# Performance work log

Hardware: AMD Instinct MI355X
Metric: run time of the kernel (lower is better)

Reference implementation:

```python
import jax, jax.numpy as jnp
import numpy as np

N_CELLS = 50000
IN_DIM = 2000
H_DIM = 128
Z_DIM = 64
N_PROTO = 32
N_CLASSES = 8
B = 64  # number of samples (ragged groups)


def _xavier(key, shape):
    fan_out, fan_in = shape
    std = jnp.sqrt(2.0 / (fan_in + fan_out))
    return std * jax.random.normal(key, shape, dtype=jnp.float32)


def setup_inputs() -> dict:
    key = jax.random.key(0)
    ks = jax.random.split(key, 16)
    x = jax.random.normal(ks[0], (N_CELLS, IN_DIM), dtype=jnp.float32)
    y = jax.random.randint(ks[1], (B,), 0, N_CLASSES)
    # sorted segment ids emulating split_idx over B ragged groups; every group non-empty
    seg = jnp.sort(jax.random.randint(ks[2], (N_CELLS - B,), 0, B))
    segment_ids = jnp.sort(jnp.concatenate([jnp.arange(B, dtype=seg.dtype), seg])).astype(jnp.int32)
    return {
        "x": x,
        "y": y,
        "segment_ids": segment_ids,
        "enc_i_w": _xavier(ks[3], (H_DIM, IN_DIM)),
        "enc_i_b": jnp.zeros((H_DIM,), jnp.float32),
        "enc_h0_w": _xavier(ks[4], (H_DIM, H_DIM)),
        "enc_h0_b": jnp.zeros((H_DIM,), jnp.float32),
        "enc_z_w": _xavier(ks[5], (Z_DIM, H_DIM)),
        "enc_z_b": jnp.zeros((Z_DIM,), jnp.float32),
        "imp_i_w": _xavier(ks[6], (H_DIM, IN_DIM)),
        "imp_i_b": jnp.zeros((H_DIM,), jnp.float32),
        "imp_h0_w": _xavier(ks[7], (H_DIM, H_DIM)),
        "imp_h0_b": jnp.zeros((H_DIM,), jnp.float32),
        "imp_p_w": _xavier(ks[8], (N_PROTO * N_CLASSES, H_DIM)),
        "imp_p_b": jnp.zeros((N_PROTO * N_CLASSES,), jnp.float32),
        "prototypes": _xavier(ks[9], (N_PROTO, Z_DIM)),
    }


def _linear(x, w, b):
    # torch nn.Linear: y = x @ w.T + b
    return x @ w.T + b


def reference(x, y, segment_ids,
              enc_i_w, enc_i_b, enc_h0_w, enc_h0_b, enc_z_w, enc_z_b,
              imp_i_w, imp_i_b, imp_h0_w, imp_h0_b, imp_p_w, imp_p_b,
              prototypes):
    act = jax.nn.leaky_relu  # slope 0.01, matches nn.LeakyReLU default
    # encode
    h = act(_linear(x, enc_i_w, enc_i_b))
    h = act(_linear(h, enc_h0_w, enc_h0_b))
    z = act(_linear(h, enc_z_w, enc_z_b))  # [N, Z]
    # importance scores
    hi = act(_linear(x, imp_i_w, imp_i_b))
    hi = act(_linear(hi, imp_h0_w, imp_h0_b))
    imp = jax.nn.sigmoid(_linear(hi, imp_p_w, imp_p_b)).reshape(-1, N_PROTO, N_CLASSES)  # [N, P, C]
    # squared euclidean cell-to-prototype distances [N, P]
    c2p = jnp.sum((z[:, None, :] - prototypes[None, :, :]) ** 2, axis=-1)
    sim = 1.0 / (c2p + 0.5)  # [N, P]
    c_logits = jnp.einsum('np,npc->nc', sim, imp)  # [N, C]
    # ragged per-sample mean (segment mean over split_idx groups)
    sums = jax.ops.segment_sum(c_logits, segment_ids, num_segments=B)
    counts = jax.ops.segment_sum(jnp.ones((c_logits.shape[0],), c_logits.dtype), segment_ids, num_segments=B)
    logits = sums / counts[:, None]  # [B, C]
    # mean cross-entropy
    logp = jax.nn.log_softmax(logits, axis=-1)
    clf_loss = -jnp.mean(jnp.take_along_axis(logp, y[:, None], axis=1))
    total_loss = clf_loss  # ct is None -> ct_loss = 0
    return total_loss, logits
```

## Files before the change

### kernel.cpp

```cpp
#include <hip/hip_runtime.h>
#include <math.h>

#define N_CELLS 50000
#define KDIM    2000
#define KPAD    2048
#define BK      128
#define NCHUNK  16
#define TM      64

typedef unsigned short u16;
typedef unsigned int   u32;
typedef __attribute__((ext_vector_type(8))) short          bf16x8;
typedef __attribute__((ext_vector_type(4))) float          f32x4;
typedef __attribute__((ext_vector_type(4))) unsigned short u16x4;

__device__ __forceinline__ u16 f2bf(float f) {
  u32 u = __builtin_bit_cast(u32, f);
  return (u16)((u + 0x7FFFu + ((u >> 16) & 1u)) >> 16);
}
__device__ __forceinline__ float bf2f(u16 h) {
  u32 u = ((u32)h) << 16;
  return __builtin_bit_cast(float, u);
}

#define WS_W1     0
#define WS_W2     1048576
#define WS_W3     (WS_W2 + 65536)
#define WS_PT     (WS_W3 + 81920)
#define WS_PN     (WS_PT + 4096)
#define WS_B1     (WS_PN + 128)
#define WS_B2     (WS_B1 + 1024)
#define WS_B3     (WS_B2 + 1024)
#define WS_SEGSUM (WS_B3 + 1280)
#define WS_SEGCNT (WS_SEGSUM + 2048)

#define LDS_SEG  0
#define LDS_SA   256
#define LDS_H2   256
#define LDS_SIM  256
#define LDS_H1   34048
#define LDS_IMP  34048
#define LDS_ZB   67840
#define LDS_CL   67840
#define LDS_ZN   77056
#define LDS_TOTAL 77312

__global__ void __launch_bounds__(256) convert_kernel(
    const float* __restrict__ enc_i_w, const float* __restrict__ imp_i_w,
    const float* __restrict__ enc_h0_w, const float* __restrict__ imp_h0_w,
    const float* __restrict__ enc_z_w, const float* __restrict__ imp_p_w,
    const float* __restrict__ protos,
    const float* __restrict__ enc_i_b, const float* __restrict__ imp_i_b,
    const float* __restrict__ enc_h0_b, const float* __restrict__ imp_h0_b,
    const float* __restrict__ enc_z_b, const float* __restrict__ imp_p_b,
    char* __restrict__ ws)
{
  u16* W1 = (u16*)(ws + WS_W1);
  u16* W2 = (u16*)(ws + WS_W2);
  u16* W3 = (u16*)(ws + WS_W3);
  u16* PT = (u16*)(ws + WS_PT);
  float* PN = (float*)(ws + WS_PN);
  float* b1 = (float*)(ws + WS_B1);
  float* b2 = (float*)(ws + WS_B2);
  float* b3 = (float*)(ws + WS_B3);

  int idx = blockIdx.x * 256 + threadIdx.x;
  if (idx < 524288) {
    int r = idx >> 11, k = idx & 2047;
    float v = 0.f;
    if (k < KDIM) v = (r < 128) ? enc_i_w[r * KDIM + k] : imp_i_w[(r - 128) * KDIM + k];
    W1[((k >> 3) * 256 + r) * 8 + (k & 7)] = f2bf(v);
  } else if (idx < 557056) {
    int j = idx - 524288; int r = j >> 7, k = j & 127;
    float v = (r < 128) ? enc_h0_w[r * 128 + k] : imp_h0_w[(r - 128) * 128 + k];
    W2[j] = f2bf(v);
  } else if (idx < 598016) {
    int j = idx - 557056; int r = j >> 7, k = j & 127;
    float v = (r < 64) ? enc_z_w[r * 128 + k] : imp_p_w[(r - 64) * 128 + k];
    W3[j] = f2bf(v);
  } else if (idx < 600064) {
    int j = idx - 598016;
    PT[j] = f2bf(protos[j]);
  } else if (idx < 600096) {
    int p = idx - 600064;
    float s = 0.f;
    for (int d = 0; d < 64; ++d) { float pb = bf2f(f2bf(protos[p * 64 + d])); s += pb * pb; }
    PN[p] = s + 0.5f;
  } else if (idx < 600352) {
    int j = idx - 600096;
    b1[j] = (j < 128) ? enc_i_b[j] : imp_i_b[j - 128];
  } else if (idx < 600608) {
    int j = idx - 600352;
    b2[j] = (j < 128) ? enc_h0_b[j] : imp_h0_b[j - 128];
  } else if (idx < 600928) {
    int j = idx - 600608;
    b3[j] = (j < 64) ? enc_z_b[j] : imp_p_b[j - 64];
  }
}

#define MFMA(a, b, c) __builtin_amdgcn_mfma_f32_16x16x32_bf16((a), (b), (c), 0, 0, 0)
#define LD8(p) (*(const bf16x8*)(const void*)(p))

#define A_GLOAD(t_) {                                                        \
  const int kb_ = (t_) * BK;                                                 \
  _Pragma("unroll")                                                          \
  for (int j_ = 0; j_ < 4; ++j_) {                                           \
    const int col_ = kb_ + (ac + 8 * j_) * 4;                                \
    aR[j_] = (arow_ok && col_ < KDIM)                                        \
               ? __builtin_nontemporal_load((const f32x4*)(xr + col_))       \
               : f4z;                                                        \
  } }

#define A_STORE(buf_) {                                                      \
  u16* da_ = saB + (buf_) * (TM * BK) + ar * BK;                             \
  _Pragma("unroll")                                                          \
  for (int j_ = 0; j_ < 4; ++j_) {                                           \
    u16x4 pk_;                                                               \
    pk_[0] = f2bf(aR[j_][0]); pk_[1] = f2bf(aR[j_][1]);                      \
    pk_[2] = f2bf(aR[j_][2]); pk_[3] = f2bf(aR[j_][3]);                      \
    const int cu_ = ((ac + 8 * j_) * 4) ^ swW;                               \
    *(u16x4*)(void*)(da_ + cu_) = pk_;                                       \
  } }

__global__ void __launch_bounds__(512, 4) fused_main(
    const float* __restrict__ x, const int* __restrict__ seg,
    const char* __restrict__ ws,
    float* __restrict__ seg_sums, float* __restrict__ seg_counts)
{
  extern __shared__ char smem[];
  const int tid  = threadIdx.x;
  const int wave = tid >> 6;
  const int lane = tid & 63;
  const int l15  = lane & 15;
  const int l4   = lane >> 4;
  const int row0 = blockIdx.x * TM;
  int valid = N_CELLS - row0; if (valid > TM) valid = TM;
  const int wn0 = wave * 32;

  if (tid < TM) {
    int r = row0 + tid;
    ((int*)(smem + LDS_SEG))[tid] = (r < N_CELLS) ? seg[r] : 0;
  }

  u16* const saB = (u16*)(smem + LDS_SA);
  const int ar = tid >> 3;
  const int ac = tid & 7;
  const bool arow_ok = (row0 + ar) < N_CELLS;
  const float* xr = x + (size_t)(arow_ok ? (row0 + ar) : 0) * KDIM;
  const u16* const w1t = (const u16*)(ws + WS_W1);
  const u16* const bbase = w1t + (size_t)(l4 * 256 + wn0 + l15) * 8;
  const int swW = (ar & 7) << 3;
  const int swR = (l15 & 7) << 3;
  const f32x4 f4z = (f32x4){0.f, 0.f, 0.f, 0.f};

  f32x4 aR[4];
  f32x4 acc1[4][2];
#pragma unroll
  for (int m = 0; m < 4; ++m)
#pragma unroll
    for (int n = 0; n < 2; ++n) acc1[m][n] = (f32x4){0.f, 0.f, 0.f, 0.f};

  A_GLOAD(0);
  A_STORE(0);
  __syncthreads();

  int cur = 0;
  for (int t = 0; t < NCHUNK; ++t) {
    bf16x8 bR[8];
#pragma unroll
    for (int q = 0; q < 8; ++q)
      bR[q] = LD8(bbase + (size_t)(t * 16 + (q >> 1) * 4) * 2048 + (q & 1) * 128);
    if (t + 1 < NCHUNK) A_GLOAD(t + 1);
    const u16* sa = saB + cur * (TM * BK);
#pragma unroll
    for (int kk = 0; kk < 4; ++kk) {
      const int co = (kk * 32 + l4 * 8) ^ swR;
      bf16x8 af0 = LD8(sa + (l15)      * BK + co);
      bf16x8 af1 = LD8(sa + (16 + l15) * BK + co);
      bf16x8 af2 = LD8(sa + (32 + l15) * BK + co);
      bf16x8 af3 = LD8(sa + (48 + l15) * BK + co);
      acc1[0][0] = MFMA(af0, bR[kk*2+0], acc1[0][0]);
      acc1[0][1] = MFMA(af0, bR[kk*2+1], acc1[0][1]);
      acc1[1][0] = MFMA(af1, bR[kk*2+0], acc1[1][0]);
      acc1[1][1] = MFMA(af1, bR[kk*2+1], acc1[1][1]);
      acc1[2][0] = MFMA(af2, bR[kk*2+0], acc1[2][0]);
      acc1[2][1] = MFMA(af2, bR[kk*2+1], acc1[2][1]);
      acc1[3][0] = MFMA(af3, bR[kk*2+0], acc1[3][0]);
      acc1[3][1] = MFMA(af3, bR[kk*2+1], acc1[3][1]);
    }
    if (t + 1 < NCHUNK) A_STORE(cur ^ 1);
    __syncthreads();
    cur ^= 1;
  }

  u16* h1 = (u16*)(smem + LDS_H1);
  {
    const float* b1 = (const float*)(ws + WS_B1);
#pragma unroll
    for (int n = 0; n < 2; ++n) {
      const int col = wn0 + n * 16 + l15;
      const float bias = b1[col];
#pragma unroll
      for (int m = 0; m < 4; ++m)
#pragma unroll
        for (int j = 0; j < 4; ++j) {
          const int row = m * 16 + l4 * 4 + j;
          float v = acc1[m][n][j] + bias;
          v = (v > 0.f) ? v : 0.01f * v;
          h1[row * 264 + col] = f2bf(v);
        }
    }
  }
  __syncthreads();

  u16* h2 = (u16*)(smem + LDS_H2);
  {
    const u16* W2 = (const u16*)(ws + WS_W2);
    const int branch = wave >> 2;
    f32x4 acc2[4][2];
#pragma unroll
    for (int m = 0; m < 4; ++m)
#pragma unroll
      for (int n = 0; n < 2; ++n) acc2[m][n] = (f32x4){0.f, 0.f, 0.f, 0.f};
#pragma unroll
    for (int kk = 0; kk < 4; ++kk) {
      const int ko = kk * 32 + l4 * 8;
      bf16x8 af[4], bfr[2];
#pragma unroll
      for (int m = 0; m < 4; ++m) af[m] = LD8(h1 + (m * 16 + l15) * 264 + branch * 128 + ko);
#pragma unroll
      for (int n = 0; n < 2; ++n) bfr[n] = LD8(W2 + (wn0 + n * 16 + l15) * 128 + ko);
#pragma unroll
      for (int m = 0; m < 4; ++m)
#pragma unroll
        for (int n = 0; n < 2; ++n) acc2[m][n] = MFMA(af[m], bfr[n], acc2[m][n]);
    }
    const float* b2 = (const float*)(ws + WS_B2);
#pragma unroll
    for (int n = 0; n < 2; ++n) {
      const int col = wn0 + n * 16 + l15;
      const float bias = b2[col];
#pragma unroll
      for (int m = 0; m < 4; ++m)
#pragma unroll
        for (int j = 0; j < 4; ++j) {
          const int row = m * 16 + l4 * 4 + j;
          float v = acc2[m][n][j] + bias;
          v = (v > 0.f) ? v : 0.01f * v;
          h2[row * 264 + col] = f2bf(v);
        }
    }
  }
  __syncthreads();

  {
    const u16* W3 = (const u16*)(ws + WS_W3);
    const float* b3 = (const float*)(ws + WS_B3);
    f32x4 acc3[4][2];
#pragma unroll
    for (int m = 0; m < 4; ++m)
#pragma unroll
      for (int n = 0; n < 2; ++n) acc3[m][n] = (f32x4){0.f, 0.f, 0.f, 0.f};
#pragma unroll
    for (int kk = 0; kk < 4; ++kk) {
      const int ko = kk * 32 + l4 * 8;
      bf16x8 af[4], bfr[2];
#pragma unroll
      for (int m = 0; m < 4; ++m) af[m] = LD8(h2 + (m * 16 + l15) * 264 + 128 + ko);
#pragma unroll
      for (int n = 0; n < 2; ++n) bfr[n] = LD8(W3 + (64 + wn0 + n * 16 + l15) * 128 + ko);
#pragma unroll
      for (int m = 0; m < 4; ++m)
#pragma unroll
        for (int n = 0; n < 2; ++n) acc3[m][n] = MFMA(af[m], bfr[n], acc3[m][n]);
    }
    u16* impL = (u16*)(smem + LDS_IMP);
#pragma unroll
    for (int n = 0; n < 2; ++n) {
      const int col = wn0 + n * 16 + l15;
      const float bias = b3[64 + col];
#pragma unroll
      for (int m = 0; m < 4; ++m)
#pragma unroll
        for (int j = 0; j < 4; ++j) {
          const int row = m * 16 + l4 * 4 + j;
          float v = acc3[m][n][j] + bias;
          impL[row * 264 + col] = f2bf(1.f / (1.f + expf(-v)));
        }
    }
    if (wave < 4) {
      f32x4 accz[4];
#pragma unroll
      for (int n = 0; n < 4; ++n) accz[n] = (f32x4){0.f, 0.f, 0.f, 0.f};
#pragma unroll
      for (int kk = 0; kk < 4; ++kk) {
        const int ko = kk * 32 + l4 * 8;
        bf16x8 a = LD8(h2 + (wave * 16 + l15) * 264 + ko);
#pragma unroll
        for (int n = 0; n < 4; ++n) {
          bf16x8 b = LD8(W3 + (n * 16 + l15) * 128 + ko);
          accz[n] = MFMA(a, b, accz[n]);
        }
      }
      u16* zb = (u16*)(smem + LDS_ZB);
      float zn[4] = {0.f, 0.f, 0.f, 0.f};
#pragma unroll
      for (int n = 0; n < 4; ++n) {
        const int col = n * 16 + l15;
        const float bias = b3[col];
#pragma unroll
        for (int j = 0; j < 4; ++j) {
          const int row = wave * 16 + l4 * 4 + j;
          float v = accz[n][j] + bias;
          v = (v > 0.f) ? v : 0.01f * v;
          zb[row * 72 + col] = f2bf(v);
          zn[j] += v * v;
        }
      }
#pragma unroll
      for (int j = 0; j < 4; ++j) {
        float v = zn[j];
        v += __shfl_xor(v, 1); v += __shfl_xor(v, 2);
        v += __shfl_xor(v, 4); v += __shfl_xor(v, 8);
        zn[j] = v;
      }
      if (l15 == 0) {
        float* znL = (float*)(smem + LDS_ZN);
#pragma unroll
        for (int j = 0; j < 4; ++j) znL[wave * 16 + l4 * 4 + j] = zn[j];
      }
    }
  }
  __syncthreads();

  if (wave < 4) {
    const u16* zb = (const u16*)(smem + LDS_ZB);
    const u16* PT = (const u16*)(ws + WS_PT);
    const float* PN = (const float*)(ws + WS_PN);
    f32x4 accs[2];
#pragma unroll
    for (int n = 0; n < 2; ++n) accs[n] = (f32x4){0.f, 0.f, 0.f, 0.f};
#pragma unroll
    for (int kk = 0; kk < 2; ++kk) {
      const int ko = kk * 32 + l4 * 8;
      bf16x8 a = LD8(zb + (wave * 16 + l15) * 72 + ko);
#pragma unroll
      for (int n = 0; n < 2; ++n) {
        bf16x8 b = LD8(PT + (n * 16 + l15) * 64 + ko);
        accs[n] = MFMA(a, b, accs[n]);
      }
    }
    const float* znL = (const float*)(smem + LDS_ZN);
    float* simL = (float*)(smem + LDS_SIM);
#pragma unroll
    for (int n = 0; n < 2; ++n) {
      const int p = n * 16 + l15;
      const float pn = PN[p];
#pragma unroll
      for (int j = 0; j < 4; ++j) {
        const int row = wave * 16 + l4 * 4 + j;
        simL[row * 33 + p] = 1.f / (znL[row] - 2.f * accs[n][j] + pn);
      }
    }
  }
  __syncthreads();

  {
    const int r = tid >> 3, c = tid & 7;
    float* cl = (float*)(smem + LDS_CL);
    if (r < valid) {
      const float* simL = (const float*)(smem + LDS_SIM);
      const u16*  impL = (const u16*)(smem + LDS_IMP);
      float s = 0.f;
#pragma unroll
      for (int p = 0; p < 32; ++p) s += simL[r * 33 + p] * bf2f(impL[r * 264 + p * 8 + c]);
      cl[r * 8 + c] = s;
    }
    __syncthreads();
    if (r < valid) {
      const int* segL = (const int*)(smem + LDS_SEG);
      const int sg = segL[r];
      if (r == 0 || segL[r - 1] != sg) {
        float s = 0.f;
        int rr = r;
        do { s += cl[rr * 8 + c]; ++rr; } while (rr < valid && segL[rr] == sg);
        atomicAdd(&seg_sums[sg * 8 + c], s);
        if (c == 0) atomicAdd(&seg_counts[sg], (float)(rr - r));
      }
    }
  }
}

__global__ void __launch_bounds__(64) finalize_kernel(const char* __restrict__ ws,
                                                      const int* __restrict__ y,
                                                      float* __restrict__ out)
{
  const int b = threadIdx.x;
  const float* sums = (const float*)(ws + WS_SEGSUM);
  const float* cnts = (const float*)(ws + WS_SEGCNT);
  const float inv = 1.f / cnts[b];
  float lg[8];
  float m = -1e30f;
#pragma unroll
  for (int c = 0; c < 8; ++c) { lg[c] = sums[b * 8 + c] * inv; m = fmaxf(m, lg[c]); }
  float se = 0.f;
#pragma unroll
  for (int c = 0; c < 8; ++c) se += expf(lg[c] - m);
  const float lse = m + logf(se);
#pragma unroll
  for (int c = 0; c < 8; ++c) out[1 + b * 8 + c] = lg[c];
  const int yb = y[b];
  float part = -(lg[yb] - lse);
  for (int o = 1; o < 64; o <<= 1) part += __shfl_xor(part, o);
  if (b == 0) out[0] = part * (1.f / 64.f);
}

extern "C" void kernel_launch(void* const* d_in, const int* in_sizes, int n_in,
                              void* d_out, int out_size, void* d_ws, size_t ws_size,
                              hipStream_t stream)
{
  const float* x        = (const float*)d_in[0];
  const int*   y        = (const int*)d_in[1];
  const int*   seg      = (const int*)d_in[2];
  const float* enc_i_w  = (const float*)d_in[3];
  const float* enc_i_b  = (const float*)d_in[4];
  const float* enc_h0_w = (const float*)d_in[5];
  const float* enc_h0_b = (const float*)d_in[6];
  const float* enc_z_w  = (const float*)d_in[7];
  const float* enc_z_b  = (const float*)d_in[8];
  const float* imp_i_w  = (const float*)d_in[9];
  const float* imp_i_b  = (const float*)d_in[10];
  const float* imp_h0_w = (const float*)d_in[11];
  const float* imp_h0_b = (const float*)d_in[12];
  const float* imp_p_w  = (const float*)d_in[13];
  const float* imp_p_b  = (const float*)d_in[14];
  const float* protos   = (const float*)d_in[15];
  char* ws = (char*)d_ws;

  hipMemsetAsync(ws + WS_SEGSUM, 0, 2048 + 256, stream);

  convert_kernel<<<2348, 256, 0, stream>>>(
      enc_i_w, imp_i_w, enc_h0_w, imp_h0_w, enc_z_w, imp_p_w, protos,
      enc_i_b, imp_i_b, enc_h0_b, imp_h0_b, enc_z_b, imp_p_b, ws);

  const int nblocks = (N_CELLS + TM - 1) / TM;
  fused_main<<<nblocks, 512, LDS_TOTAL, stream>>>(
      x, seg, ws, (float*)(ws + WS_SEGSUM), (float*)(ws + WS_SEGCNT));

  finalize_kernel<<<1, 64, 0, stream>>>(ws, y, (float*)d_out);
}
```

Baseline: 170.1 us.

## Use persistent blocks with atomic tile scheduler and deeper A prefetch

Replaces the one-block-per-tile launch with a fixed grid of 512 persistent blocks that pull 64-row tiles from a global atomic counter. The first GEMM's K loop is unrolled by two, with two register sets for x chunks so the global loads run two chunks ahead of the MFMA work. The aim is to cut block launch and tail overhead and hide more HBM latency on the bandwidth-bound x stream. In exchange it adds an atomic plus a barrier per tile, more registers, and dynamic tile assignment that can leave load imbalance at the end.

```diff
diff --git a/kernel.cpp b/kernel.cpp
--- a/kernel.cpp
+++ b/kernel.cpp
@@ -7,6 +7,8 @@
 #define BK      128
 #define NCHUNK  16
 #define TM      64
+#define NTILES  782
+#define GRID    512
 
 typedef unsigned short u16;
 typedef unsigned int   u32;
@@ -33,6 +35,7 @@
 #define WS_B3     (WS_B2 + 1024)
 #define WS_SEGSUM (WS_B3 + 1280)
 #define WS_SEGCNT (WS_SEGSUM + 2048)
+#define WS_CTR    (WS_SEGCNT + 256)
 
 #define LDS_SEG  0
 #define LDS_SA   256
@@ -43,7 +46,8 @@
 #define LDS_ZB   67840
 #define LDS_CL   67840
 #define LDS_ZN   77056
-#define LDS_TOTAL 77312
+#define LDS_TIL  77312
+#define LDS_TOTAL 77376
 
 __global__ void __launch_bounds__(256) convert_kernel(
     const float* __restrict__ enc_i_w, const float* __restrict__ imp_i_w,
@@ -101,30 +105,56 @@
 #define MFMA(a, b, c) __builtin_amdgcn_mfma_f32_16x16x32_bf16((a), (b), (c), 0, 0, 0)
 #define LD8(p) (*(const bf16x8*)(const void*)(p))
 
-#define A_GLOAD(t_) {                                                        \
-  const int kb_ = (t_) * BK;                                                 \
+#define A_GLOAD(dst_, t_) {                                                  \
+  const int kb_ = ((t_) < NCHUNK ? (t_) : (NCHUNK - 1)) * BK;                \
   _Pragma("unroll")                                                          \
   for (int j_ = 0; j_ < 4; ++j_) {                                           \
     const int col_ = kb_ + (ac + 8 * j_) * 4;                                \
-    aR[j_] = (arow_ok && col_ < KDIM)                                        \
+    dst_[j_] = (arow_ok && col_ < KDIM)                                      \
                ? __builtin_nontemporal_load((const f32x4*)(xr + col_))       \
                : f4z;                                                        \
   } }
 
-#define A_STORE(buf_) {                                                      \
+#define A_STORE(src_, buf_) {                                                \
   u16* da_ = saB + (buf_) * (TM * BK) + ar * BK;                             \
   _Pragma("unroll")                                                          \
   for (int j_ = 0; j_ < 4; ++j_) {                                           \
     u16x4 pk_;                                                               \
-    pk_[0] = f2bf(aR[j_][0]); pk_[1] = f2bf(aR[j_][1]);                      \
-    pk_[2] = f2bf(aR[j_][2]); pk_[3] = f2bf(aR[j_][3]);                      \
+    pk_[0] = f2bf(src_[j_][0]); pk_[1] = f2bf(src_[j_][1]);                  \
+    pk_[2] = f2bf(src_[j_][2]); pk_[3] = f2bf(src_[j_][3]);                  \
     const int cu_ = ((ac + 8 * j_) * 4) ^ swW;                               \
     *(u16x4*)(void*)(da_ + cu_) = pk_;                                       \
   } }
 
+#define BLOAD(t_) {                                                          \
+  const int tc_ = (t_);                                                      \
+  _Pragma("unroll")                                                          \
+  for (int q_ = 0; q_ < 8; ++q_)                                             \
+    bR[q_] = LD8(bbase + (size_t)(tc_ * 16 + (q_ >> 1) * 4) * 2048 +         \
+                 (q_ & 1) * 128);                                            \
+  }
+
+#define G1_MFMA(saP_) {                                                      \
+  _Pragma("unroll")                                                          \
+  for (int kk_ = 0; kk_ < 4; ++kk_) {                                        \
+    const int co_ = (kk_ * 32 + l4 * 8) ^ swR;                               \
+    bf16x8 af0 = LD8((saP_) + (l15)      * BK + co_);                        \
+    bf16x8 af1 = LD8((saP_) + (16 + l15) * BK + co_);                        \
+    bf16x8 af2 = LD8((saP_) + (32 + l15) * BK + co_);                        \
+    bf16x8 af3 = LD8((saP_) + (48 + l15) * BK + co_);                        \
+    acc1[0][0] = MFMA(af0, bR[kk_*2+0], acc1[0][0]);                         \
+    acc1[0][1] = MFMA(af0, bR[kk_*2+1], acc1[0][1]);                         \
+    acc1[1][0] = MFMA(af1, bR[kk_*2+0], acc1[1][0]);                         \
+    acc1[1][1] = MFMA(af1, bR[kk_*2+1], acc1[1][1]);                         \
+    acc1[2][0] = MFMA(af2, bR[kk_*2+0], acc1[2][0]);                         \
+    acc1[2][1] = MFMA(af2, bR[kk_*2+1], acc1[2][1]);                         \
+    acc1[3][0] = MFMA(af3, bR[kk_*2+0], acc1[3][0]);                         \
+    acc1[3][1] = MFMA(af3, bR[kk_*2+1], acc1[3][1]);                         \
+  } }
+
 __global__ void __launch_bounds__(512, 4) fused_main(
     const float* __restrict__ x, const int* __restrict__ seg,
-    const char* __restrict__ ws,
+    const char* __restrict__ ws, int* __restrict__ tile_ctr,
     float* __restrict__ seg_sums, float* __restrict__ seg_counts)
 {
   extern __shared__ char smem[];
@@ -133,259 +163,256 @@
   const int lane = tid & 63;
   const int l15  = lane & 15;
   const int l4   = lane >> 4;
-  const int row0 = blockIdx.x * TM;
-  int valid = N_CELLS - row0; if (valid > TM) valid = TM;
-  const int wn0 = wave * 32;
-
-  if (tid < TM) {
-    int r = row0 + tid;
-    ((int*)(smem + LDS_SEG))[tid] = (r < N_CELLS) ? seg[r] : 0;
-  }
-
-  u16* const saB = (u16*)(smem + LDS_SA);
+  const int wn0  = wave * 32;
   const int ar = tid >> 3;
   const int ac = tid & 7;
-  const bool arow_ok = (row0 + ar) < N_CELLS;
-  const float* xr = x + (size_t)(arow_ok ? (row0 + ar) : 0) * KDIM;
-  const u16* const w1t = (const u16*)(ws + WS_W1);
-  const u16* const bbase = w1t + (size_t)(l4 * 256 + wn0 + l15) * 8;
   const int swW = (ar & 7) << 3;
   const int swR = (l15 & 7) << 3;
   const f32x4 f4z = (f32x4){0.f, 0.f, 0.f, 0.f};
 
-  f32x4 aR[4];
-  f32x4 acc1[4][2];
-#pragma unroll
-  for (int m = 0; m < 4; ++m)
-#pragma unroll
-    for (int n = 0; n < 2; ++n) acc1[m][n] = (f32x4){0.f, 0.f, 0.f, 0.f};
-
-  A_GLOAD(0);
-  A_STORE(0);
-  __syncthreads();
-
-  int cur = 0;
-  for (int t = 0; t < NCHUNK; ++t) {
+  u16* const saB = (u16*)(smem + LDS_SA);
+  const u16* const w1t = (const u16*)(ws + WS_W1);
+  const u16* const bbase = w1t + (size_t)(l4 * 256 + wn0 + l15) * 8;
+  int* const tilSh = (int*)(smem + LDS_TIL);
+
+  for (;;) {
+    if (tid == 0) *tilSh = atomicAdd(tile_ctr, 1);
+    __syncthreads();
+    const int tile = *tilSh;
+    if (tile >= NTILES) break;
+
+    const int row0 = tile * TM;
+    int valid = N_CELLS - row0; if (valid > TM) valid = TM;
+    const bool arow_ok = (row0 + ar) < N_CELLS;
+    const float* xr = x + (size_t)(arow_ok ? (row0 + ar) : 0) * KDIM;
+
+    if (tid < TM) {
+      int r = row0 + tid;
+      ((int*)(smem + LDS_SEG))[tid] = (r < N_CELLS) ? seg[r] : 0;
+    }
+
+    f32x4 aRA[4], aRB[4];
     bf16x8 bR[8];
-#pragma unroll
-    for (int q = 0; q < 8; ++q)
-      bR[q] = LD8(bbase + (size_t)(t * 16 + (q >> 1) * 4) * 2048 + (q & 1) * 128);
-    if (t + 1 < NCHUNK) A_GLOAD(t + 1);
-    const u16* sa = saB + cur * (TM * BK);
-#pragma unroll
-    for (int kk = 0; kk < 4; ++kk) {
-      const int co = (kk * 32 + l4 * 8) ^ swR;
-      bf16x8 af0 = LD8(sa + (l15)      * BK + co);
-      bf16x8 af1 = LD8(sa + (16 + l15) * BK + co);
-      bf16x8 af2 = LD8(sa + (32 + l15) * BK + co);
-      bf16x8 af3 = LD8(sa + (48 + l15) * BK + co);
-      acc1[0][0] = MFMA(af0, bR[kk*2+0], acc1[0][0]);
-      acc1[0][1] = MFMA(af0, bR[kk*2+1], acc1[0][1]);
-      acc1[1][0] = MFMA(af1, bR[kk*2+0], acc1[1][0]);
-      acc1[1][1] = MFMA(af1, bR[kk*2+1], acc1[1][1]);
-      acc1[2][0] = MFMA(af2, bR[kk*2+0], acc1[2][0]);
-      acc1[2][1] = MFMA(af2, bR[kk*2+1], acc1[2][1]);
-      acc1[3][0] = MFMA(af3, bR[kk*2+0], acc1[3][0]);
-      acc1[3][1] = MFMA(af3, bR[kk*2+1], acc1[3][1]);
-    }
-    if (t + 1 < NCHUNK) A_STORE(cur ^ 1);
-    __syncthreads();
-    cur ^= 1;
-  }
-
-  u16* h1 = (u16*)(smem + LDS_H1);
-  {
-    const float* b1 = (const float*)(ws + WS_B1);
-#pragma unroll
-    for (int n = 0; n < 2; ++n) {
-      const int col = wn0 + n * 16 + l15;
-      const float bias = b1[col];
+    f32x4 acc1[4][2];
+#pragma unroll
+    for (int m = 0; m < 4; ++m)
+#pragma unroll
+      for (int n = 0; n < 2; ++n) acc1[m][n] = (f32x4){0.f, 0.f, 0.f, 0.f};
+
+    A_GLOAD(aRA, 0);
+    A_GLOAD(aRB, 1);
+    A_STORE(aRA, 0);
+    __syncthreads();
+
+    for (int t = 0; t < NCHUNK; t += 2) {
+      BLOAD(t);
+      A_GLOAD(aRA, t + 2);
+      G1_MFMA(saB);
+      A_STORE(aRB, 1);
+      __syncthreads();
+      BLOAD(t + 1);
+      A_GLOAD(aRB, t + 3);
+      G1_MFMA(saB + TM * BK);
+      if (t + 2 < NCHUNK) {
+        A_STORE(aRA, 0);
+      }
+      __syncthreads();
+    }
+
+    u16* h1 = (u16*)(smem + LDS_H1);
+    {
+      const float* b1 = (const float*)(ws + WS_B1);
+#pragma unroll
+      for (int n = 0; n < 2; ++n) {
+        const int col = wn0 + n * 16 + l15;
+        const float bias = b1[col];
+#pragma unroll
+        for (int m = 0; m < 4; ++m)
+#pragma unroll
+          for (int j = 0; j < 4; ++j) {
+            const int row = m * 16 + l4 * 4 + j;
+            float v = acc1[m][n][j] + bias;
+            v = (v > 0.f) ? v : 0.01f * v;
+            h1[row * 264 + col] = f2bf(v);
+          }
+      }
+    }
+    __syncthreads();
+
+    u16* h2 = (u16*)(smem + LDS_H2);
+    {
+      const u16* W2 = (const u16*)(ws + WS_W2);
+      const int branch = wave >> 2;
+      f32x4 acc2[4][2];
 #pragma unroll
       for (int m = 0; m < 4; ++m)
 #pragma unroll
-        for (int j = 0; j < 4; ++j) {
-          const int row = m * 16 + l4 * 4 + j;
-          float v = acc1[m][n][j] + bias;
-          v = (v > 0.f) ? v : 0.01f * v;
-          h1[row * 264 + col] = f2bf(v);
-        }
-    }
-  }
-  __syncthreads();
-
-  u16* h2 = (u16*)(smem + LDS_H2);
-  {
-    const u16* W2 = (const u16*)(ws + WS_W2);
-    const int branch = wave >> 2;
-    f32x4 acc2[4][2];
-#pragma unroll
-    for (int m = 0; m < 4; ++m)
-#pragma unroll
-      for (int n = 0; n < 2; ++n) acc2[m][n] = (f32x4){0.f, 0.f, 0.f, 0.f};
-#pragma unroll
-    for (int kk = 0; kk < 4; ++kk) {
-      const int ko = kk * 32 + l4 * 8;
-      bf16x8 af[4], bfr[2];
-#pragma unroll
-      for (int m = 0; m < 4; ++m) af[m] = LD8(h1 + (m * 16 + l15) * 264 + branch * 128 + ko);
-#pragma unroll
-      for (int n = 0; n < 2; ++n) bfr[n] = LD8(W2 + (wn0 + n * 16 + l15) * 128 + ko);
-#pragma unroll
-      for (int m = 0; m < 4; ++m)
-#pragma unroll
-        for (int n = 0; n < 2; ++n) acc2[m][n] = MFMA(af[m], bfr[n], acc2[m][n]);
-    }
-    const float* b2 = (const float*)(ws + WS_B2);
-#pragma unroll
-    for (int n = 0; n < 2; ++n) {
-      const int col = wn0 + n * 16 + l15;
-      const float bias = b2[col];
-#pragma unroll
-      for (int m = 0; m < 4; ++m)
-#pragma unroll
-        for (int j = 0; j < 4; ++j) {
-          const int row = m * 16 + l4 * 4 + j;
-          float v = acc2[m][n][j] + bias;
-          v = (v > 0.f) ? v : 0.01f * v;
-          h2[row * 264 + col] = f2bf(v);
-        }
-    }
-  }
-  __syncthreads();
-
-  {
-    const u16* W3 = (const u16*)(ws + WS_W3);
-    const float* b3 = (const float*)(ws + WS_B3);
-    f32x4 acc3[4][2];
-#pragma unroll
-    for (int m = 0; m < 4; ++m)
-#pragma unroll
-      for (int n = 0; n < 2; ++n) acc3[m][n] = (f32x4){0.f, 0.f, 0.f, 0.f};
-#pragma unroll
-    for (int kk = 0; kk < 4; ++kk) {
-      const int ko = kk * 32 + l4 * 8;
-      bf16x8 af[4], bfr[2];
-#pragma unroll
-      for (int m = 0; m < 4; ++m) af[m] = LD8(h2 + (m * 16 + l15) * 264 + 128 + ko);
-#pragma unroll
-      for (int n = 0; n < 2; ++n) bfr[n] = LD8(W3 + (64 + wn0 + n * 16 + l15) * 128 + ko);
-#pragma unroll
-      for (int m = 0; m < 4; ++m)
-#pragma unroll
-        for (int n = 0; n < 2; ++n) acc3[m][n] = MFMA(af[m], bfr[n], acc3[m][n]);
-    }
-    u16* impL = (u16*)(smem + LDS_IMP);
-#pragma unroll
-    for (int n = 0; n < 2; ++n) {
-      const int col = wn0 + n * 16 + l15;
-      const float bias = b3[64 + col];
-#pragma unroll
-      for (int m = 0; m < 4; ++m)
-#pragma unroll
-        for (int j = 0; j < 4; ++j) {
-          const int row = m * 16 + l4 * 4 + j;
-          float v = acc3[m][n][j] + bias;
-          impL[row * 264 + col] = f2bf(1.f / (1.f + expf(-v)));
-        }
-    }
-    if (wave < 4) {
-      f32x4 accz[4];
-#pragma unroll
-      for (int n = 0; n < 4; ++n) accz[n] = (f32x4){0.f, 0.f, 0.f, 0.f};
+        for (int n = 0; n < 2; ++n) acc2[m][n] = (f32x4){0.f, 0.f, 0.f, 0.f};
 #pragma unroll
       for (int kk = 0; kk < 4; ++kk) {
         const int ko = kk * 32 + l4 * 8;
-        bf16x8 a = LD8(h2 + (wave * 16 + l15) * 264 + ko);
+        bf16x8 af[4], bfr[2];
+#pragma unroll
+        for (int m = 0; m < 4; ++m) af[m] = LD8(h1 + (m * 16 + l15) * 264 + branch * 128 + ko);
+#pragma unroll
+        for (int n = 0; n < 2; ++n) bfr[n] = LD8(W2 + (wn0 + n * 16 + l15) * 128 + ko);
+#pragma unroll
+        for (int m = 0; m < 4; ++m)
+#pragma unroll
+          for (int n = 0; n < 2; ++n) acc2[m][n] = MFMA(af[m], bfr[n], acc2[m][n]);
+      }
+      const float* b2 = (const float*)(ws + WS_B2);
+#pragma unroll
+      for (int n = 0; n < 2; ++n) {
+        const int col = wn0 + n * 16 + l15;
+        const float bias = b2[col];
+#pragma unroll
+        for (int m = 0; m < 4; ++m)
+#pragma unroll
+          for (int j = 0; j < 4; ++j) {
+            const int row = m * 16 + l4 * 4 + j;
+            float v = acc2[m][n][j] + bias;
+            v = (v > 0.f) ? v : 0.01f * v;
+            h2[row * 264 + col] = f2bf(v);
+          }
+      }
+    }
+    __syncthreads();
+
+    {
+      const u16* W3 = (const u16*)(ws + WS_W3);
+      const float* b3 = (const float*)(ws + WS_B3);
+      f32x4 acc3[4][2];
+#pragma unroll
+      for (int m = 0; m < 4; ++m)
+#pragma unroll
+        for (int n = 0; n < 2; ++n) acc3[m][n] = (f32x4){0.f, 0.f, 0.f, 0.f};
+#pragma unroll
+      for (int kk = 0; kk < 4; ++kk) {
+        const int ko = kk * 32 + l4 * 8;
+        bf16x8 af[4], bfr[2];
+#pragma unroll
+        for (int m = 0; m < 4; ++m) af[m] = LD8(h2 + (m * 16 + l15) * 264 + 128 + ko);
+#pragma unroll
+        for (int n = 0; n < 2; ++n) bfr[n] = LD8(W3 + (64 + wn0 + n * 16 + l15) * 128 + ko);
+#pragma unroll
+        for (int m = 0; m < 4; ++m)
+#pragma unroll
+          for (int n = 0; n < 2; ++n) acc3[m][n] = MFMA(af[m], bfr[n], acc3[m][n]);
+      }
+      u16* impL = (u16*)(smem + LDS_IMP);
+#pragma unroll
+      for (int n = 0; n < 2; ++n) {
+        const int col = wn0 + n * 16 + l15;
+        const float bias = b3[64 + col];
+#pragma unroll
+        for (int m = 0; m < 4; ++m)
+#pragma unroll
+          for (int j = 0; j < 4; ++j) {
+            const int row = m * 16 + l4 * 4 + j;
+            float v = acc3[m][n][j] + bias;
+            impL[row * 264 + col] = f2bf(1.f / (1.f + expf(-v)));
+          }
+      }
+      if (wave < 4) {
+        f32x4 accz[4];
+#pragma unroll
+        for (int n = 0; n < 4; ++n) accz[n] = (f32x4){0.f, 0.f, 0.f, 0.f};
+#pragma unroll
+        for (int kk = 0; kk < 4; ++kk) {
+          const int ko = kk * 32 + l4 * 8;
+          bf16x8 a = LD8(h2 + (wave * 16 + l15) * 264 + ko);
+#pragma unroll
+          for (int n = 0; n < 4; ++n) {
+            bf16x8 b = LD8(W3 + (n * 16 + l15) * 128 + ko);
+            accz[n] = MFMA(a, b, accz[n]);
+          }
+        }
+        u16* zb = (u16*)(smem + LDS_ZB);
+        float zn[4] = {0.f, 0.f, 0.f, 0.f};
 #pragma unroll
         for (int n = 0; n < 4; ++n) {
-          bf16x8 b = LD8(W3 + (n * 16 + l15) * 128 + ko);
-          accz[n] = MFMA(a, b, accz[n]);
-        }
-      }
-      u16* zb = (u16*)(smem + LDS_ZB);
-      float zn[4] = {0.f, 0.f, 0.f, 0.f};
-#pragma unroll
-      for (int n = 0; n < 4; ++n) {
-        const int col = n * 16 + l15;
-        const float bias = b3[col];
+          const int col = n * 16 + l15;
+          const float bias = b3[col];
+#pragma unroll
+          for (int j = 0; j < 4; ++j) {
+            const int row = wave * 16 + l4 * 4 + j;
+            float v = accz[n][j] + bias;
+            v = (v > 0.f) ? v : 0.01f * v;
+            zb[row * 72 + col] = f2bf(v);
+            zn[j] += v * v;
+          }
+        }
+#pragma unroll
+        for (int j = 0; j < 4; ++j) {
+          float v = zn[j];
+          v += __shfl_xor(v, 1); v += __shfl_xor(v, 2);
+          v += __shfl_xor(v, 4); v += __shfl_xor(v, 8);
+          zn[j] = v;
+        }
+        if (l15 == 0) {
+          float* znL = (float*)(smem + LDS_ZN);
+#pragma unroll
+          for (int j = 0; j < 4; ++j) znL[wave * 16 + l4 * 4 + j] = zn[j];
+        }
+      }
+    }
+    __syncthreads();
+
+    if (wave < 4) {
+      const u16* zb = (const u16*)(smem + LDS_ZB);
+      const u16* PT = (const u16*)(ws + WS_PT);
+      const float* PN = (const float*)(ws + WS_PN);
+      f32x4 accs[2];
+#pragma unroll
+      for (int n = 0; n < 2; ++n) accs[n] = (f32x4){0.f, 0.f, 0.f, 0.f};
+#pragma unroll
+      for (int kk = 0; kk < 2; ++kk) {
+        const int ko = kk * 32 + l4 * 8;
+        bf16x8 a = LD8(zb + (wave * 16 + l15) * 72 + ko);
+#pragma unroll
+        for (int n = 0; n < 2; ++n) {
+          bf16x8 b = LD8(PT + (n * 16 + l15) * 64 + ko);
+          accs[n] = MFMA(a, b, accs[n]);
+        }
+      }
+      const float* znL = (const float*)(smem + LDS_ZN);
+      float* simL = (float*)(smem + LDS_SIM);
+#pragma unroll
+      for (int n = 0; n < 2; ++n) {
+        const int p = n * 16 + l15;
+        const float pn = PN[p];
 #pragma unroll
         for (int j = 0; j < 4; ++j) {
           const int row = wave * 16 + l4 * 4 + j;
-          float v = accz[n][j] + bias;
-          v = (v > 0.f) ? v : 0.01f * v;
-          zb[row * 72 + col] = f2bf(v);
-          zn[j] += v * v;
-        }
-      }
-#pragma unroll
-      for (int j = 0; j < 4; ++j) {
-        float v = zn[j];
-        v += __shfl_xor(v, 1); v += __shfl_xor(v, 2);
-        v += __shfl_xor(v, 4); v += __shfl_xor(v, 8);
-        zn[j] = v;
-      }
-      if (l15 == 0) {
-        float* znL = (float*)(smem + LDS_ZN);
-#pragma unroll
-        for (int j = 0; j < 4; ++j) znL[wave * 16 + l4 * 4 + j] = zn[j];
-      }
-    }
-  }
-  __syncthreads();
-
-  if (wave < 4) {
-    const u16* zb = (const u16*)(smem + LDS_ZB);
-    const u16* PT = (const u16*)(ws + WS_PT);
-    const float* PN = (const float*)(ws + WS_PN);
-    f32x4 accs[2];
-#pragma unroll
-    for (int n = 0; n < 2; ++n) accs[n] = (f32x4){0.f, 0.f, 0.f, 0.f};
-#pragma unroll
-    for (int kk = 0; kk < 2; ++kk) {
-      const int ko = kk * 32 + l4 * 8;
-      bf16x8 a = LD8(zb + (wave * 16 + l15) * 72 + ko);
-#pragma unroll
-      for (int n = 0; n < 2; ++n) {
-        bf16x8 b = LD8(PT + (n * 16 + l15) * 64 + ko);
-        accs[n] = MFMA(a, b, accs[n]);
-      }
-    }
-    const float* znL = (const float*)(smem + LDS_ZN);
-    float* simL = (float*)(smem + LDS_SIM);
-#pragma unroll
-    for (int n = 0; n < 2; ++n) {
-      const int p = n * 16 + l15;
-      const float pn = PN[p];
-#pragma unroll
-      for (int j = 0; j < 4; ++j) {
-        const int row = wave * 16 + l4 * 4 + j;
-        simL[row * 33 + p] = 1.f / (znL[row] - 2.f * accs[n][j] + pn);
-      }
-    }
-  }
-  __syncthreads();
-
-  {
-    const int r = tid >> 3, c = tid & 7;
-    float* cl = (float*)(smem + LDS_CL);
-    if (r < valid) {
-      const float* simL = (const float*)(smem + LDS_SIM);
-      const u16*  impL = (const u16*)(smem + LDS_IMP);
-      float s = 0.f;
-#pragma unroll
-      for (int p = 0; p < 32; ++p) s += simL[r * 33 + p] * bf2f(impL[r * 264 + p * 8 + c]);
-      cl[r * 8 + c] = s;
-    }
-    __syncthreads();
-    if (r < valid) {
-      const int* segL = (const int*)(smem + LDS_SEG);
-      const int sg = segL[r];
-      if (r == 0 || segL[r - 1] != sg) {
+          simL[row * 33 + p] = 1.f / (znL[row] - 2.f * accs[n][j] + pn);
+        }
+      }
+    }
+    __syncthreads();
+
+    {
+      const int r = tid >> 3, c = tid & 7;
+      float* cl = (float*)(smem + LDS_CL);
+      if (r < valid) {
+        const float* simL = (const float*)(smem + LDS_SIM);
+        const u16*  impL = (const u16*)(smem + LDS_IMP);
         float s = 0.f;
-        int rr = r;
-        do { s += cl[rr * 8 + c]; ++rr; } while (rr < valid && segL[rr] == sg);
-        atomicAdd(&seg_sums[sg * 8 + c], s);
-        if (c == 0) atomicAdd(&seg_counts[sg], (float)(rr - r));
+#pragma unroll
+        for (int p = 0; p < 32; ++p) s += simL[r * 33 + p] * bf2f(impL[r * 264 + p * 8 + c]);
+        cl[r * 8 + c] = s;
+      }
+      __syncthreads();
+      if (r < valid) {
+        const int* segL = (const int*)(smem + LDS_SEG);
+        const int sg = segL[r];
+        if (r == 0 || segL[r - 1] != sg) {
+          float s = 0.f;
+          int rr = r;
+          do { s += cl[rr * 8 + c]; ++rr; } while (rr < valid && segL[rr] == sg);
+          atomicAdd(&seg_sums[sg * 8 + c], s);
+          if (c == 0) atomicAdd(&seg_counts[sg], (float)(rr - r));
+        }
       }
     }
   }
@@ -437,15 +464,15 @@
   const float* protos   = (const float*)d_in[15];
   char* ws = (char*)d_ws;
 
-  hipMemsetAsync(ws + WS_SEGSUM, 0, 2048 + 256, stream);
+  hipMemsetAsync(ws + WS_SEGSUM, 0, 2048 + 256 + 64, stream);
 
   convert_kernel<<<2348, 256, 0, stream>>>(
       enc_i_w, imp_i_w, enc_h0_w, imp_h0_w, enc_z_w, imp_p_w, protos,
       enc_i_b, imp_i_b, enc_h0_b, imp_h0_b, enc_z_b, imp_p_b, ws);
 
-  const int nblocks = (N_CELLS + TM - 1) / TM;
-  fused_main<<<nblocks, 512, LDS_TOTAL, stream>>>(
-      x, seg, ws, (float*)(ws + WS_SEGSUM), (float*)(ws + WS_SEGCNT));
+  fused_main<<<GRID, 512, LDS_TOTAL, stream>>>(
+      x, seg, ws, (int*)(ws + WS_CTR),
+      (float*)(ws + WS_SEGSUM), (float*)(ws + WS_SEGCNT));
 
   finalize_kernel<<<1, 64, 0, stream>>>(ws, y, (float*)d_out);
 }
```

Measured after the change: 253.8 us. 49.2% more time.
